# Kernel optimization log

Measured on AMD Instinct MI355X. Metric: run time of the kernel, lower is better.

## Reference

```python
import jax, jax.numpy as jnp
import numpy as np

BINS = 256
RMIN, RMAX = 0.0, 1.0


def _histc(x):
    # torch.histc semantics: values in [min, max] are binned; x == max falls in last bin;
    # values outside the range are ignored.
    xf = x.reshape(-1)
    scale = BINS / (RMAX - RMIN)
    idx = jnp.clip(jnp.floor((xf - RMIN) * scale).astype(jnp.int32), 0, BINS - 1)
    valid = ((xf >= RMIN) & (xf <= RMAX)).astype(x.dtype)
    return jax.ops.segment_sum(valid, idx, num_segments=BINS)


def setup_inputs() -> dict:
    key = jax.random.key(0)
    k1, k2 = jax.random.split(key)
    img1 = jax.random.uniform(k1, (32, 3, 512, 512), dtype=jnp.float32)
    img2 = jax.random.uniform(k2, (32, 3, 512, 512), dtype=jnp.float32)
    return {"img1": img1, "img2": img2}


def reference(img1, img2):
    hist1 = _histc(img1)
    hist2 = _histc(img2)
    # norm=True
    hist1 = hist1 / jnp.sum(hist1)
    hist2 = hist2 / jnp.sum(hist2)
    loss = jnp.sum(jnp.abs(hist1 - hist2))
    # reduction='mean'
    return loss / BINS
```

## Files before the change

kernel.cpp:

```cpp
#include <hip/hip_runtime.h>

#define BINS  256
#define NCOPY 8
#define BLOCK 512
#define HALFT 256
#define GRID  1024

typedef unsigned int u32;
typedef unsigned long long u64;

__device__ __forceinline__ void gbin1(float x, u32* g) {
    if (x >= 0.0f && x <= 1.0f) {
        u32 bin = (u32)(x * 256.0f);
        bin = bin > 255u ? 255u : bin;
        atomicAdd(&g[bin], 1u);
    }
}
__device__ __forceinline__ void gbin4(float4 v, u32* g) {
    gbin1(v.x, g); gbin1(v.y, g); gbin1(v.z, g); gbin1(v.w, g);
}

__device__ __forceinline__ void dbin(float x, u32* hc) {
    if (x >= 0.0f && x <= 1.0f) {
        u32 bin = (u32)(x * 256.0f);
        bin = bin > 255u ? 255u : bin;
        atomicAdd(&hc[bin * NCOPY], 1u);
    }
}

__device__ __forceinline__ void bs_round(float x, const u32 e[6], u32 cnt[4])
{
    u64 ge, le, b0, b1, b2, b3, b4, b5, b6, b7;
    u32 vb, t0, t1;
    asm("v_mul_f32 %[vb], 0x43800000, %[x]\n\t"
        "v_cvt_u32_f32 %[vb], %[vb]\n\t"
        "v_min_u32 %[vb], 0xff, %[vb]\n\t"
        "v_cmp_ge_f32 %[ge], %[x], 0\n\t"
        "v_cmp_le_f32 %[le], %[x], 1.0\n\t"
        "v_lshlrev_b32 %[t0], 31, %[vb]\n\t"
        "v_cmp_lt_i32 %[b0], %[t0], 0\n\t"
        "v_lshlrev_b32 %[t1], 30, %[vb]\n\t"
        "v_cmp_lt_i32 %[b1], %[t1], 0\n\t"
        "v_lshlrev_b32 %[t0], 29, %[vb]\n\t"
        "v_cmp_lt_i32 %[b2], %[t0], 0\n\t"
        "v_lshlrev_b32 %[t1], 28, %[vb]\n\t"
        "v_cmp_lt_i32 %[b3], %[t1], 0\n\t"
        "v_lshlrev_b32 %[t0], 27, %[vb]\n\t"
        "v_cmp_lt_i32 %[b4], %[t0], 0\n\t"
        "v_lshlrev_b32 %[t1], 26, %[vb]\n\t"
        "v_cmp_lt_i32 %[b5], %[t1], 0\n\t"
        "v_lshlrev_b32 %[t0], 25, %[vb]\n\t"
        "v_cmp_lt_i32 %[b6], %[t0], 0\n\t"
        "v_lshlrev_b32 %[t1], 24, %[vb]\n\t"
        "v_cmp_lt_i32 %[b7], %[t1], 0"
        : [ge] "=&s"(ge), [le] "=&s"(le),
          [b0] "=&s"(b0), [b1] "=&s"(b1), [b2] "=&s"(b2), [b3] "=&s"(b3),
          [b4] "=&s"(b4), [b5] "=&s"(b5), [b6] "=&s"(b6), [b7] "=&s"(b7),
          [vb] "=&v"(vb), [t0] "=&v"(t0), [t1] "=&v"(t1)
        : [x] "v"(x));

    const u64 mv = ge & le;

    u32 aLo = (u32)mv
            & (((u32)b2) ^ e[0]) & (((u32)b3) ^ e[1]) & (((u32)b4) ^ e[2])
            & (((u32)b5) ^ e[3]) & (((u32)b6) ^ e[4]) & (((u32)b7) ^ e[5]);
    u32 aHi = (u32)(mv >> 32)
            & (((u32)(b2 >> 32)) ^ e[0]) & (((u32)(b3 >> 32)) ^ e[1])
            & (((u32)(b4 >> 32)) ^ e[2]) & (((u32)(b5 >> 32)) ^ e[3])
            & (((u32)(b6 >> 32)) ^ e[4]) & (((u32)(b7 >> 32)) ^ e[5]);

    const u64 c00 = ~(b0 | b1);
    const u64 c01 = b0 & ~b1;
    const u64 c10 = ~b0 & b1;
    const u64 c11 = b0 & b1;
    cnt[0] += __popc(aLo & (u32)c00) + __popc(aHi & (u32)(c00 >> 32));
    cnt[1] += __popc(aLo & (u32)c01) + __popc(aHi & (u32)(c01 >> 32));
    cnt[2] += __popc(aLo & (u32)c10) + __popc(aHi & (u32)(c10 >> 32));
    cnt[3] += __popc(aLo & (u32)c11) + __popc(aHi & (u32)(c11 >> 32));
}

__device__ __forceinline__ void bs4(float4 v, const u32 e[6], u32 cnt[4])
{
    bs_round(v.x, e, cnt);
    bs_round(v.y, e, cnt);
    bs_round(v.z, e, cnt);
    bs_round(v.w, e, cnt);
}

__global__ __launch_bounds__(BLOCK, 8) void hist_kernel(
    const float* __restrict__ img1, const float* __restrict__ img2,
    u32* __restrict__ g_h1, u32* __restrict__ g_h2,
    long long n)
{
    __shared__ u32 lh[2][BINS][NCOPY];

    const int tid  = threadIdx.x;
    const int lane = tid & 63;
    const int copy = tid & (NCOPY - 1);

    for (int k = tid; k < 2 * BINS * NCOPY; k += BLOCK)
        ((u32*)lh)[k] = 0u;
    __syncthreads();

    u32 cnt1[4] = {0u, 0u, 0u, 0u};
    u32 cnt2[4] = {0u, 0u, 0u, 0u};
    u32* h1c = &lh[0][0][copy];
    u32* h2c = &lh[1][0][copy];

    const long long n4 = n >> 2;
    const long long S  = (long long)gridDim.x * HALFT;
    const long long tripsTot = n4 / S;
    const long long tripsB = tripsTot / 2;
    const long long tripsD = tripsTot - tripsB;
    const long long QB = tripsB * S;
    const long long uniform_end = QB + tripsD * S;

    const float4* p1 = (const float4*)img1;
    const float4* p2 = (const float4*)img2;

    if (tid < HALFT) {
        u32 e[6];
#pragma unroll
        for (int k = 0; k < 6; ++k)
            e[k] = ((lane >> k) & 1) ? 0u : 0xFFFFFFFFu;

        long long i = (long long)blockIdx.x * HALFT + tid;
        if (tripsB >= 2) {
            float4 a0 = p1[i],  b0 = p2[i];
            long long ii = i + S;
            float4 a1 = p1[ii], b1 = p2[ii];
            for (long long t = 0; t + 2 < tripsB; ++t) {
                const long long in = ii + S;
                float4 a2 = p1[in], b2v = p2[in];
                bs4(a0, e, cnt1); bs4(b0, e, cnt2);
                a0 = a1; b0 = b1; a1 = a2; b1 = b2v; ii = in;
            }
            bs4(a0, e, cnt1); bs4(b0, e, cnt2);
            bs4(a1, e, cnt1); bs4(b1, e, cnt2);
        } else if (tripsB == 1) {
            float4 a0 = p1[i], b0 = p2[i];
            bs4(a0, e, cnt1); bs4(b0, e, cnt2);
        }
    } else {
        long long i = QB + (long long)blockIdx.x * HALFT + (tid - HALFT);
        if (tripsD >= 2) {
            float4 a0 = p1[i],  b0 = p2[i];
            long long ii = i + S;
            float4 a1 = p1[ii], b1 = p2[ii];
            for (long long t = 0; t + 2 < tripsD; ++t) {
                const long long in = ii + S;
                float4 a2 = p1[in], b2v = p2[in];
                dbin(a0.x, h1c); dbin(a0.y, h1c); dbin(a0.z, h1c); dbin(a0.w, h1c);
                dbin(b0.x, h2c); dbin(b0.y, h2c); dbin(b0.z, h2c); dbin(b0.w, h2c);
                a0 = a1; b0 = b1; a1 = a2; b1 = b2v; ii = in;
            }
            dbin(a0.x, h1c); dbin(a0.y, h1c); dbin(a0.z, h1c); dbin(a0.w, h1c);
            dbin(b0.x, h2c); dbin(b0.y, h2c); dbin(b0.z, h2c); dbin(b0.w, h2c);
            dbin(a1.x, h1c); dbin(a1.y, h1c); dbin(a1.z, h1c); dbin(a1.w, h1c);
            dbin(b1.x, h2c); dbin(b1.y, h2c); dbin(b1.z, h2c); dbin(b1.w, h2c);
        } else if (tripsD == 1) {
            float4 a0 = p1[i], b0 = p2[i];
            dbin(a0.x, h1c); dbin(a0.y, h1c); dbin(a0.z, h1c); dbin(a0.w, h1c);
            dbin(b0.x, h2c); dbin(b0.y, h2c); dbin(b0.z, h2c); dbin(b0.w, h2c);
        }
    }

    {
        const long long gtid = (long long)blockIdx.x * BLOCK + tid;
        const long long nthr = (long long)gridDim.x * BLOCK;
        for (long long q = uniform_end + gtid; q < n4; q += nthr) {
            gbin4(p1[q], g_h1);
            gbin4(p2[q], g_h2);
        }
        for (long long k2 = (n4 << 2) + gtid; k2 < n; k2 += nthr) {
            gbin1(img1[k2], g_h1);
            gbin1(img2[k2], g_h2);
        }
    }

    __syncthreads();
#pragma unroll
    for (int j = 0; j < 4; ++j) {
        if (cnt1[j]) atomicAdd(&lh[0][4 * lane + j][copy], cnt1[j]);
        if (cnt2[j]) atomicAdd(&lh[1][4 * lane + j][copy], cnt2[j]);
    }
    __syncthreads();

    for (int b = tid; b < BINS; b += BLOCK) {
        u32 s1 = 0u, s2 = 0u;
#pragma unroll
        for (int c = 0; c < NCOPY; ++c) { s1 += lh[0][b][c]; s2 += lh[1][b][c]; }
        if (s1) atomicAdd(&g_h1[b], s1);
        if (s2) atomicAdd(&g_h2[b], s2);
    }
}

__global__ __launch_bounds__(BINS) void finalize_kernel(
    const u32* __restrict__ h1, const u32* __restrict__ h2,
    float* __restrict__ out)
{
    const int tid = threadIdx.x;
    const u32 c1 = h1[tid];
    const u32 c2 = h2[tid];

    __shared__ u32 s1[4], s2[4];
    __shared__ double sd[4];

    u32 r1 = c1, r2 = c2;
#pragma unroll
    for (int off = 32; off > 0; off >>= 1) {
        r1 += __shfl_down(r1, off);
        r2 += __shfl_down(r2, off);
    }
    if ((tid & 63) == 0) { s1[tid >> 6] = r1; s2[tid >> 6] = r2; }
    __syncthreads();

    const double N1 = (double)(s1[0] + s1[1] + s1[2] + s1[3]);
    const double N2 = (double)(s2[0] + s2[1] + s2[2] + s2[3]);

    double d = fabs((double)c1 / N1 - (double)c2 / N2);
#pragma unroll
    for (int off = 32; off > 0; off >>= 1)
        d += __shfl_down(d, off);
    if ((tid & 63) == 0) sd[tid >> 6] = d;
    __syncthreads();

    if (tid == 0) {
        double tot = sd[0] + sd[1] + sd[2] + sd[3];
        out[0] = (float)(tot / (double)BINS);
    }
}

extern "C" void kernel_launch(void* const* d_in, const int* in_sizes, int n_in,
                              void* d_out, int out_size, void* d_ws, size_t ws_size,
                              hipStream_t stream) {
    const float* img1 = (const float*)d_in[0];
    const float* img2 = (const float*)d_in[1];
    const long long n = (long long)in_sizes[0];

    u32* g_h1 = (u32*)d_ws;
    u32* g_h2 = g_h1 + BINS;

    hipMemsetAsync(d_ws, 0, 2 * BINS * sizeof(u32), stream);

    hist_kernel<<<GRID, BLOCK, 0, stream>>>(img1, img2, g_h1, g_h2, n);
    finalize_kernel<<<1, BINS, 0, stream>>>(g_h1, g_h2, (float*)d_out);
}
```

Baseline: 61.80 us.

## Add third worker group binning into replicated global histograms

Each block is split three ways: 256 threads keep the bit-sliced counting path, 192 use shared-memory atomics, and 64 threads atomically add into 32 replicated global histogram copies. The work ratios are rebalanced so all three paths share the load, and the finalize kernel sums the global copies. The tail loop now uses the shared-memory atomics instead of global atomics. This aims to spread the binning load over more hardware units (bit-slice ALU, LDS atomics, L2 atomics), at the cost of L2 atomic traffic and a larger memset.

```diff
diff --git a/kernel.cpp b/kernel.cpp
--- a/kernel.cpp
+++ b/kernel.cpp
@@ -3,28 +3,29 @@
 #define BINS  256
 #define NCOPY 8
 #define BLOCK 512
-#define HALFT 256
 #define GRID  1024
+#define GCOPY 32
+
+#define NB 256
+#define ND 192
+#define NG 64
 
 typedef unsigned int u32;
 typedef unsigned long long u64;
-
-__device__ __forceinline__ void gbin1(float x, u32* g) {
-    if (x >= 0.0f && x <= 1.0f) {
-        u32 bin = (u32)(x * 256.0f);
-        bin = bin > 255u ? 255u : bin;
-        atomicAdd(&g[bin], 1u);
-    }
-}
-__device__ __forceinline__ void gbin4(float4 v, u32* g) {
-    gbin1(v.x, g); gbin1(v.y, g); gbin1(v.z, g); gbin1(v.w, g);
-}
 
 __device__ __forceinline__ void dbin(float x, u32* hc) {
     if (x >= 0.0f && x <= 1.0f) {
         u32 bin = (u32)(x * 256.0f);
         bin = bin > 255u ? 255u : bin;
         atomicAdd(&hc[bin * NCOPY], 1u);
+    }
+}
+
+__device__ __forceinline__ void gbin_c(float x, u32* gc) {
+    if (x >= 0.0f && x <= 1.0f) {
+        u32 bin = (u32)(x * 256.0f);
+        bin = bin > 255u ? 255u : bin;
+        atomicAdd(&gc[bin], 1u);
     }
 }
 
@@ -90,7 +91,8 @@
 __global__ __launch_bounds__(BLOCK, 8) void hist_kernel(
     const float* __restrict__ img1, const float* __restrict__ img2,
     u32* __restrict__ g_h1, u32* __restrict__ g_h2,
-    long long n)
+    u32* __restrict__ gcop,
+    int g_on, long long n)
 {
     __shared__ u32 lh[2][BINS][NCOPY];
 
@@ -108,29 +110,40 @@
     u32* h2c = &lh[1][0][copy];
 
     const long long n4 = n >> 2;
-    const long long S  = (long long)gridDim.x * HALFT;
-    const long long tripsTot = n4 / S;
-    const long long tripsB = tripsTot / 2;
-    const long long tripsD = tripsTot - tripsB;
-    const long long QB = tripsB * S;
-    const long long uniform_end = QB + tripsD * S;
+    const long long unit = (long long)GRID * NG;
+    const long long units = n4 / unit;
+    const long long tripsB = units / 12;
+    long long tripsD, tripsG;
+    if (g_on) {
+        tripsD = (units * 3) / 16;
+        tripsG = units - 4 * tripsB - 3 * tripsD;
+    } else {
+        tripsD = (units - 4 * tripsB) / 3;
+        tripsG = 0;
+    }
+    const long long S_b = (long long)GRID * NB;
+    const long long S_d = (long long)GRID * ND;
+    const long long S_g = (long long)GRID * NG;
+    const long long QB = tripsB * S_b;
+    const long long QD = QB + tripsD * S_d;
+    const long long covered = QD + tripsG * S_g;
 
     const float4* p1 = (const float4*)img1;
     const float4* p2 = (const float4*)img2;
 
-    if (tid < HALFT) {
+    if (tid < NB) {
         u32 e[6];
 #pragma unroll
         for (int k = 0; k < 6; ++k)
             e[k] = ((lane >> k) & 1) ? 0u : 0xFFFFFFFFu;
 
-        long long i = (long long)blockIdx.x * HALFT + tid;
+        long long i = (long long)blockIdx.x * NB + tid;
         if (tripsB >= 2) {
             float4 a0 = p1[i],  b0 = p2[i];
-            long long ii = i + S;
+            long long ii = i + S_b;
             float4 a1 = p1[ii], b1 = p2[ii];
             for (long long t = 0; t + 2 < tripsB; ++t) {
-                const long long in = ii + S;
+                const long long in = ii + S_b;
                 float4 a2 = p1[in], b2v = p2[in];
                 bs4(a0, e, cnt1); bs4(b0, e, cnt2);
                 a0 = a1; b0 = b1; a1 = a2; b1 = b2v; ii = in;
@@ -141,14 +154,14 @@
             float4 a0 = p1[i], b0 = p2[i];
             bs4(a0, e, cnt1); bs4(b0, e, cnt2);
         }
-    } else {
-        long long i = QB + (long long)blockIdx.x * HALFT + (tid - HALFT);
+    } else if (tid < NB + ND) {
+        long long i = QB + (long long)blockIdx.x * ND + (tid - NB);
         if (tripsD >= 2) {
             float4 a0 = p1[i],  b0 = p2[i];
-            long long ii = i + S;
+            long long ii = i + S_d;
             float4 a1 = p1[ii], b1 = p2[ii];
             for (long long t = 0; t + 2 < tripsD; ++t) {
-                const long long in = ii + S;
+                const long long in = ii + S_d;
                 float4 a2 = p1[in], b2v = p2[in];
                 dbin(a0.x, h1c); dbin(a0.y, h1c); dbin(a0.z, h1c); dbin(a0.w, h1c);
                 dbin(b0.x, h2c); dbin(b0.y, h2c); dbin(b0.z, h2c); dbin(b0.w, h2c);
@@ -163,18 +176,43 @@
             dbin(a0.x, h1c); dbin(a0.y, h1c); dbin(a0.z, h1c); dbin(a0.w, h1c);
             dbin(b0.x, h2c); dbin(b0.y, h2c); dbin(b0.z, h2c); dbin(b0.w, h2c);
         }
+    } else if (tripsG > 0) {
+        u32* gc1 = gcop + (u32)(lane & (GCOPY - 1)) * 512u;
+        u32* gc2 = gc1 + 256;
+        long long i = QD + (long long)blockIdx.x * NG + (tid - NB - ND);
+        if (tripsG >= 2) {
+            float4 a0 = p1[i],  b0 = p2[i];
+            long long ii = i + S_g;
+            float4 a1 = p1[ii], b1 = p2[ii];
+            for (long long t = 0; t + 2 < tripsG; ++t) {
+                const long long in = ii + S_g;
+                float4 a2 = p1[in], b2v = p2[in];
+                gbin_c(a0.x, gc1); gbin_c(a0.y, gc1); gbin_c(a0.z, gc1); gbin_c(a0.w, gc1);
+                gbin_c(b0.x, gc2); gbin_c(b0.y, gc2); gbin_c(b0.z, gc2); gbin_c(b0.w, gc2);
+                a0 = a1; b0 = b1; a1 = a2; b1 = b2v; ii = in;
+            }
+            gbin_c(a0.x, gc1); gbin_c(a0.y, gc1); gbin_c(a0.z, gc1); gbin_c(a0.w, gc1);
+            gbin_c(b0.x, gc2); gbin_c(b0.y, gc2); gbin_c(b0.z, gc2); gbin_c(b0.w, gc2);
+            gbin_c(a1.x, gc1); gbin_c(a1.y, gc1); gbin_c(a1.z, gc1); gbin_c(a1.w, gc1);
+            gbin_c(b1.x, gc2); gbin_c(b1.y, gc2); gbin_c(b1.z, gc2); gbin_c(b1.w, gc2);
+        } else {
+            float4 a0 = p1[i], b0 = p2[i];
+            gbin_c(a0.x, gc1); gbin_c(a0.y, gc1); gbin_c(a0.z, gc1); gbin_c(a0.w, gc1);
+            gbin_c(b0.x, gc2); gbin_c(b0.y, gc2); gbin_c(b0.z, gc2); gbin_c(b0.w, gc2);
+        }
     }
 
     {
         const long long gtid = (long long)blockIdx.x * BLOCK + tid;
-        const long long nthr = (long long)gridDim.x * BLOCK;
-        for (long long q = uniform_end + gtid; q < n4; q += nthr) {
-            gbin4(p1[q], g_h1);
-            gbin4(p2[q], g_h2);
+        const long long nthr = (long long)GRID * BLOCK;
+        for (long long q = covered + gtid; q < n4; q += nthr) {
+            float4 a = p1[q], b = p2[q];
+            dbin(a.x, h1c); dbin(a.y, h1c); dbin(a.z, h1c); dbin(a.w, h1c);
+            dbin(b.x, h2c); dbin(b.y, h2c); dbin(b.z, h2c); dbin(b.w, h2c);
         }
         for (long long k2 = (n4 << 2) + gtid; k2 < n; k2 += nthr) {
-            gbin1(img1[k2], g_h1);
-            gbin1(img2[k2], g_h2);
+            dbin(img1[k2], h1c);
+            dbin(img2[k2], h2c);
         }
     }
 
@@ -197,11 +235,19 @@
 
 __global__ __launch_bounds__(BINS) void finalize_kernel(
     const u32* __restrict__ h1, const u32* __restrict__ h2,
+    const u32* __restrict__ gcop, int g_on,
     float* __restrict__ out)
 {
     const int tid = threadIdx.x;
-    const u32 c1 = h1[tid];
-    const u32 c2 = h2[tid];
+    u32 c1 = h1[tid];
+    u32 c2 = h2[tid];
+    if (g_on) {
+#pragma unroll 8
+        for (int c = 0; c < GCOPY; ++c) {
+            c1 += gcop[c * 512 + tid];
+            c2 += gcop[c * 512 + 256 + tid];
+        }
+    }
 
     __shared__ u32 s1[4], s2[4];
     __shared__ double sd[4];
@@ -240,9 +286,13 @@
 
     u32* g_h1 = (u32*)d_ws;
     u32* g_h2 = g_h1 + BINS;
-
-    hipMemsetAsync(d_ws, 0, 2 * BINS * sizeof(u32), stream);
-
-    hist_kernel<<<GRID, BLOCK, 0, stream>>>(img1, img2, g_h1, g_h2, n);
-    finalize_kernel<<<1, BINS, 0, stream>>>(g_h1, g_h2, (float*)d_out);
-}
+    u32* gcop = g_h2 + BINS;
+
+    const size_t need = (size_t)(2 * BINS + GCOPY * 512) * sizeof(u32);
+    const int g_on = (ws_size >= need) ? 1 : 0;
+
+    hipMemsetAsync(d_ws, 0, g_on ? need : 2 * BINS * sizeof(u32), stream);
+
+    hist_kernel<<<GRID, BLOCK, 0, stream>>>(img1, img2, g_h1, g_h2, gcop, g_on, n);
+    finalize_kernel<<<1, BINS, 0, stream>>>(g_h1, g_h2, gcop, g_on, (float*)d_out);
+}
```

Measured after the change: 238.1 us. +285.2%, slower.
